# Performance work log

Hardware: AMD Instinct MI355X
Metric: run time of the kernel (lower is better)

## Reference

```python
import jax, jax.numpy as jnp
import numpy as np

NUM_HEADS = 16
HEAD_DIM = 64
PATCH_NUMS = [1, 2, 3, 4, 5, 6, 8, 10, 13, 16, 32]
MAX_SCALE_MUL = float(np.log(100.0))


def precompute_freqs_cis(dim, patch_nums, theta=10000.0):
    # Returns [L, dim//2, 2] (cos, sin) pairs; matches torch.polar construction.
    freqs = 1.0 / theta ** (np.arange(0, dim, 4)[: dim // 4].astype(np.float32) / dim)  # [dim//4]
    tx, ty = [], []
    grid = 32.0
    for p in patch_nums:
        ix, iy = np.meshgrid(np.arange(p), np.arange(p), indexing="ij")  # torch default 'ij'
        tx.append(ix.flatten().astype(np.float32) / p * grid)
        ty.append(iy.flatten().astype(np.float32) / p * grid)
    tx = np.concatenate(tx)
    ty = np.concatenate(ty)
    ang = np.concatenate([np.outer(tx, freqs), np.outer(ty, freqs)], axis=1).astype(np.float32)  # [L, dim//2]
    return np.stack([np.cos(ang), np.sin(ang)], axis=-1)  # [L, dim//2, 2]


FREQS_CIS_CROSS = jnp.asarray(precompute_freqs_cis(HEAD_DIM, [12]))  # [144, 32, 2]


def _rope(x, cis):
    # x: [B, H, S, D]; cis: [S, D//2, 2] -> complex multiply on (even, odd) pairs.
    B, H, S, D = x.shape
    xr = x.reshape(B, H, S, D // 2, 2)
    a, b = xr[..., 0], xr[..., 1]
    c = cis[..., 0][None, None]  # [1,1,S,D//2]
    d = cis[..., 1][None, None]
    return jnp.stack([a * c - b * d, a * d + b * c], axis=-1).reshape(B, H, S, D)


def setup_inputs() -> dict:
    key = jax.random.key(0)
    ks = jax.random.split(key, 6)
    B, C, Ck, Lk = 8, 1024, 1024, 144
    fc = precompute_freqs_cis(HEAD_DIM, PATCH_NUMS)
    L = fc.shape[0]  # 1704
    return {
        "x": jax.random.normal(ks[0], (B, L, C), jnp.float32),
        "y": jax.random.normal(ks[1], (B, Lk, Ck), jnp.float32),
        "freqs_cis": jnp.asarray(fc),
        "attn_bias": jax.random.normal(ks[2], (1, 1, L, Lk), jnp.float32) * 0.1,
        "Wq": jax.random.normal(ks[3], (C, C), jnp.float32) * 0.02,
        "q_bias": jnp.zeros((C,), jnp.float32),
        "Wkv": jax.random.normal(ks[4], (2 * C, Ck), jnp.float32) * 0.02,
        "v_bias": jnp.zeros((C,), jnp.float32),
        "Wproj": jax.random.normal(ks[5], (C, C), jnp.float32) * 0.02,
        "b_proj": jnp.zeros((C,), jnp.float32),
        "scale_mul": jnp.full((1, NUM_HEADS, 1, 1), np.log(4.0), jnp.float32),
    }


def reference(x, y, freqs_cis, attn_bias, Wq, q_bias, Wkv, v_bias, Wproj, b_proj, scale_mul):
    B, L, C = x.shape
    H, D = NUM_HEADS, HEAD_DIM
    Lk = y.shape[1]
    # fused QKV projections (k bias is the zero buffer)
    q = (x @ Wq.T + q_bias).reshape(B, L, H, D).transpose(0, 2, 1, 3)  # [B,H,L,D]
    kv_bias = jnp.concatenate([jnp.zeros_like(v_bias), v_bias])
    kv = (y @ Wkv.T + kv_bias).reshape(B, Lk, 2, H, D)
    k = kv[:, :, 0].transpose(0, 2, 1, 3)  # [B,H,Lk,D]
    v = kv[:, :, 1].transpose(0, 2, 1, 3)
    # attn_l2_norm path: scale = 1, per-head learned multiplier
    sm = jnp.exp(jnp.minimum(scale_mul, MAX_SCALE_MUL))  # [1,H,1,1]
    q = q / jnp.maximum(jnp.linalg.norm(q, axis=-1, keepdims=True), 1e-12) * sm
    k = k / jnp.maximum(jnp.linalg.norm(k, axis=-1, keepdims=True), 1e-12)
    # inline RoPE (cross freqs recomputed from 12x12 grid every forward in the original)
    q = _rope(q, freqs_cis)
    k = _rope(k, FREQS_CIS_CROSS)
    # manual (non-flash) masked attention, scale = 1 due to l2 norm
    logits = jnp.einsum("bhld,bhkd->bhlk", q, k) + attn_bias
    attn = jax.nn.softmax(logits, axis=-1)
    oup = jnp.einsum("bhlk,bhkd->bhld", attn, v).transpose(0, 2, 1, 3).reshape(B, L, C)
    return oup @ Wproj.T + b_proj
```

## Files before the change

### kernel.cpp

```cpp
#include <hip/hip_runtime.h>

using u16 = unsigned short;
using u32 = unsigned int;

typedef __bf16 bf16x8 __attribute__((ext_vector_type(8)));
typedef float  f32x4  __attribute__((ext_vector_type(4)));
typedef _Float16 f16;
typedef _Float16 f16x4 __attribute__((ext_vector_type(4)));
typedef _Float16 f16x8 __attribute__((ext_vector_type(8)));
typedef u16 u16x4 __attribute__((ext_vector_type(4)));

__device__ __forceinline__ float b2f(u16 u) { return __uint_as_float(((u32)u) << 16); }
__device__ __forceinline__ u16 f2b(float f) {
    u32 u = __float_as_uint(f);
    return (u16)((u + 0x7FFFu + ((u >> 16) & 1u)) >> 16);
}

__device__ __forceinline__ void async_cp16(void* lds, const void* g) {
    __builtin_amdgcn_global_load_lds(
        (const __attribute__((address_space(1))) u32*)g,
        (__attribute__((address_space(3))) u32*)lds, 16, 0, 0);
}

__global__ __launch_bounds__(256) void split_f32(const float* __restrict__ src,
                                                 u16* __restrict__ hi,
                                                 u16* __restrict__ lo, int n4) {
    int i = blockIdx.x * 256 + threadIdx.x;
    if (i >= n4) return;
    f32x4 v = reinterpret_cast<const f32x4*>(src)[i];
    u16x4 H, L;
#pragma unroll
    for (int j = 0; j < 4; j++) {
        u16 hb = f2b(v[j]);
        H[j] = hb;
        L[j] = f2b(v[j] - b2f(hb));
    }
    reinterpret_cast<u16x4*>(hi)[i] = H;
    reinterpret_cast<u16x4*>(lo)[i] = L;
}

__global__ __launch_bounds__(256) void cvt_f16(const float* __restrict__ src,
                                               f16* __restrict__ dst, int n4) {
    int i = blockIdx.x * 256 + threadIdx.x;
    if (i >= n4) return;
    f32x4 v = reinterpret_cast<const f32x4*>(src)[i];
    f16x4 h = {(f16)v[0], (f16)v[1], (f16)v[2], (f16)v[3]};
    reinterpret_cast<f16x4*>(dst)[i] = h;
}

__device__ __forceinline__ void split8(f32x4 a0, f32x4 a1, bf16x8& hi, bf16x8& lo) {
    union { bf16x8 v; u16 s[8]; } H, L;
#pragma unroll
    for (int j = 0; j < 4; j++) {
        float f = a0[j]; u16 hb = f2b(f); H.s[j] = hb;     L.s[j] = f2b(f - b2f(hb));
        float g = a1[j]; u16 gb = f2b(g); H.s[4 + j] = gb; L.s[4 + j] = f2b(g - b2f(gb));
    }
    hi = H.v; lo = L.v;
}

__global__ __launch_bounds__(512) void gemm_q(const u16* __restrict__ xhi,
                                              const u16* __restrict__ xlo,
                                              const u16* __restrict__ whi,
                                              const u16* __restrict__ wlo,
                                              const float* __restrict__ qb,
                                              const float* __restrict__ fc,
                                              const float* __restrict__ smul,
                                              f16* __restrict__ qout) {
    const int K = 1024, L = 1704;
    __shared__ u16 xs[2][2][64][64];
    int tid = threadIdx.x;
    int lane = tid & 63, wv = tid >> 6;
    int mt = blockIdx.x >> 1;
    int hg = blockIdx.x & 1;
    int h  = hg * 8 + wv;
    int lr = lane & 15, quad = lane >> 4;
    long m0 = (long)mt * 64;

    int srow = tid >> 3, scol = (tid & 7) * 8;
    const u16* g_hi = xhi + (m0 + srow) * K + scol;
    const u16* g_lo = xlo + (m0 + srow) * K + scol;
    u16* l_hi0 = &xs[0][0][srow][scol];
    u16* l_lo0 = &xs[0][1][srow][scol];
    u16* l_hi1 = &xs[1][0][srow][scol];
    u16* l_lo1 = &xs[1][1][srow][scol];

    const bf16x8* wh_p[4];
    const bf16x8* wl_p[4];
#pragma unroll
    for (int i = 0; i < 4; i++) {
        long woff = ((long)(h * 64 + i * 16 + lr)) * K;
        wh_p[i] = reinterpret_cast<const bf16x8*>(whi + woff) + quad;
        wl_p[i] = reinterpret_cast<const bf16x8*>(wlo + woff) + quad;
    }

    f32x4 acc[4][4] = {};

    async_cp16(l_hi0, g_hi);
    async_cp16(l_lo0, g_lo);
    __syncthreads();

    for (int c = 0; c < 16; c++) {
        if (c < 15) {
            const u16* gh = g_hi + (c + 1) * 64;
            const u16* gl = g_lo + (c + 1) * 64;
            if (c & 1) { async_cp16(l_hi0, gh); async_cp16(l_lo0, gl); }
            else       { async_cp16(l_hi1, gh); async_cp16(l_lo1, gl); }
        }
        int buf = c & 1;
#pragma unroll
        for (int s = 0; s < 2; s++) {
            bf16x8 AH[4], AL[4], WH[4], WL[4];
#pragma unroll
            for (int i = 0; i < 4; i++) {
                WH[i] = wh_p[i][c * 8 + s * 4];
                WL[i] = wl_p[i][c * 8 + s * 4];
            }
#pragma unroll
            for (int i = 0; i < 4; i++) {
                AH[i] = *reinterpret_cast<const bf16x8*>(&xs[buf][0][i * 16 + lr][s * 32 + quad * 8]);
                AL[i] = *reinterpret_cast<const bf16x8*>(&xs[buf][1][i * 16 + lr][s * 32 + quad * 8]);
            }
#pragma unroll
            for (int mi = 0; mi < 4; mi++)
#pragma unroll
                for (int ni = 0; ni < 4; ni++) {
                    acc[mi][ni] = __builtin_amdgcn_mfma_f32_16x16x32_bf16(AH[mi], WH[ni], acc[mi][ni], 0, 0, 0);
                    acc[mi][ni] = __builtin_amdgcn_mfma_f32_16x16x32_bf16(AL[mi], WH[ni], acc[mi][ni], 0, 0, 0);
                    acc[mi][ni] = __builtin_amdgcn_mfma_f32_16x16x32_bf16(AH[mi], WL[ni], acc[mi][ni], 0, 0, 0);
                }
        }
        __syncthreads();
    }

    float sm = __expf(fminf(smul[h], 4.6051702f));
#pragma unroll
    for (int mi = 0; mi < 4; mi++) {
#pragma unroll
        for (int r = 0; r < 4; r++) {
            long rowg = m0 + mi * 16 + quad * 4 + r;
            float v[4];
            float ss = 0.f;
#pragma unroll
            for (int ni = 0; ni < 4; ni++) {
                v[ni] = acc[mi][ni][r] + qb[h * 64 + ni * 16 + lr];
                ss += v[ni] * v[ni];
            }
            ss += __shfl_xor(ss, 1, 64); ss += __shfl_xor(ss, 2, 64);
            ss += __shfl_xor(ss, 4, 64); ss += __shfl_xor(ss, 8, 64);
            float inv = sm / fmaxf(sqrtf(ss), 1e-12f);
            int l = (int)(rowg % L);
            f16* orow = qout + rowg * 1024 + h * 64;
#pragma unroll
            for (int ni = 0; ni < 4; ni++) {
                float u = v[ni] * inv;
                int d = ni * 16 + lr;
                int j = d >> 1;
                float c = fc[(l * 32 + j) * 2];
                float s = fc[(l * 32 + j) * 2 + 1];
                float pr = __shfl_xor(u, 1, 64);
                float o = (lane & 1) ? (pr * s + u * c) : (u * c - pr * s);
                orow[d] = (f16)o;
            }
        }
    }
}

__constant__ double FREQS16[16] = {
    1.0, 0.5623413251903491, 0.31622776601683794, 0.17782794100389228,
    0.1, 0.05623413251903491, 0.03162277660168379, 0.017782794100389228,
    0.01, 0.005623413251903491, 0.0031622776601683794, 0.0017782794100389228,
    0.001, 0.0005623413251903491, 0.00031622776601683794, 0.00017782794100389228};

__global__ __launch_bounds__(256) void gemm_kv(const float* __restrict__ y,
                                               const float* __restrict__ Wkv,
                                               const float* __restrict__ vb,
                                               f16* __restrict__ khp,
                                               f16* __restrict__ klp,
                                               f16* __restrict__ vhp,
                                               f16* __restrict__ vlp) {
    const int K = 1024;
    int lane = threadIdx.x & 63, wv = threadIdx.x >> 6;
    int mt = blockIdx.x >> 3;
    int nt = (blockIdx.x & 7) * 4 + wv;
    int lr = lane & 15, quad = lane >> 4;
    long m0 = (long)mt * 64;

    const float* arow[4];
    const float* wrow[4];
#pragma unroll
    for (int i = 0; i < 4; i++) {
        arow[i] = y   + (m0 + i * 16 + lr) * K + quad * 8;
        wrow[i] = Wkv + ((long)(nt * 64 + i * 16 + lr)) * K + quad * 8;
    }

    f32x4 acc[4][4] = {};
    for (int ks = 0; ks < 32; ks++) {
        bf16x8 ah[4], al[4], wh[4], wl[4];
#pragma unroll
        for (int i = 0; i < 4; i++) {
            const float* ap = arow[i] + ks * 32;
            split8(*(const f32x4*)ap, *(const f32x4*)(ap + 4), ah[i], al[i]);
            const float* wp = wrow[i] + ks * 32;
            split8(*(const f32x4*)wp, *(const f32x4*)(wp + 4), wh[i], wl[i]);
        }
#pragma unroll
        for (int mi = 0; mi < 4; mi++)
#pragma unroll
            for (int ni = 0; ni < 4; ni++) {
                acc[mi][ni] = __builtin_amdgcn_mfma_f32_16x16x32_bf16(ah[mi], wh[ni], acc[mi][ni], 0, 0, 0);
                acc[mi][ni] = __builtin_amdgcn_mfma_f32_16x16x32_bf16(al[mi], wh[ni], acc[mi][ni], 0, 0, 0);
                acc[mi][ni] = __builtin_amdgcn_mfma_f32_16x16x32_bf16(ah[mi], wl[ni], acc[mi][ni], 0, 0, 0);
            }
    }

    bool isv = nt >= 16;
    int h = isv ? nt - 16 : nt;
#pragma unroll
    for (int mi = 0; mi < 4; mi++) {
#pragma unroll
        for (int r = 0; r < 4; r++) {
            long row = m0 + mi * 16 + quad * 4 + r;
            int b = (int)(row / 144), lk = (int)(row % 144);
            long bh = b * 16 + h;
            float v[4];
#pragma unroll
            for (int ni = 0; ni < 4; ni++)
                v[ni] = acc[mi][ni][r] + (isv ? vb[h * 64 + ni * 16 + lr] : 0.f);
            if (!isv) {
                float ss = v[0] * v[0] + v[1] * v[1] + v[2] * v[2] + v[3] * v[3];
                ss += __shfl_xor(ss, 1, 64); ss += __shfl_xor(ss, 2, 64);
                ss += __shfl_xor(ss, 4, 64); ss += __shfl_xor(ss, 8, 64);
                float inv = 1.f / fmaxf(sqrtf(ss), 1e-12f);
                f16* kh_row = khp + (bh * 144 + lk) * 64;
                f16* kl_row = klp + (bh * 144 + lk) * 64;
#pragma unroll
                for (int ni = 0; ni < 4; ni++) {
                    float u = v[ni] * inv;
                    int d = ni * 16 + lr;
                    int j = d >> 1;
                    int f = j & 15;
                    float tc = (j < 16) ? ((float)(lk / 12)) / 12.0f * 32.0f
                                        : ((float)(lk % 12)) / 12.0f * 32.0f;
                    float ang = (float)((double)tc * FREQS16[f]);
                    float c = cosf(ang), s = sinf(ang);
                    float pr = __shfl_xor(u, 1, 64);
                    float o = (lane & 1) ? (pr * s + u * c) : (u * c - pr * s);
                    f16 oh = (f16)o;
                    f16 ol = (f16)(o - (float)oh);
                    kh_row[d] = oh;
                    kl_row[d] = ol;
                }
            } else {
#pragma unroll
                for (int ni = 0; ni < 4; ni++) {
                    float val = v[ni];
                    int d = ni * 16 + lr;
                    f16 vh = (f16)val;
                    f16 vl = (f16)(val - (float)vh);
                    vhp[(bh * 64 + d) * 144 + lk] = vh;
                    vlp[(bh * 64 + d) * 144 + lk] = vl;
                }
            }
        }
    }
}

__global__ __launch_bounds__(256, 3) void attn(const f16* q,
                                               const f16* __restrict__ khp,
                                               const f16* __restrict__ klp,
                                               const f16* __restrict__ vhp,
                                               const f16* __restrict__ vlp,
                                               const float* __restrict__ abias,
                                               f16* aout) {
    const int L = 1704;
    __shared__ __align__(16) f16 ps[4][16][152];
    int tid = threadIdx.x;
    int lane = tid & 63, wv = tid >> 6;
    int lr = lane & 15, quad = lane >> 4;
    int ltile = blockIdx.x % 27;
    int bh = blockIdx.x / 27;
    int h = bh & 15, b = bh >> 4;
    int l0 = ltile * 64;
    int rows = min(64, L - l0);

    int rA = wv * 16 + lr;
    int rAc = min(rA, rows - 1);
    const f16* qrow = q + ((long)(b * L + l0 + rAc)) * 1024 + h * 64;
    f16x8 qa0 = *reinterpret_cast<const f16x8*>(qrow + quad * 8);
    f16x8 qa1 = *reinterpret_cast<const f16x8*>(qrow + 32 + quad * 8);

    const f16* khb = khp + (long)bh * (144 * 64);
    const f16* klb = klp + (long)bh * (144 * 64);

    f32x4 acc[9] = {};
#pragma unroll
    for (int t = 0; t < 9; t++) {
        const f16* k0 = khb + (t * 16 + lr) * 64 + quad * 8;
        const f16* k1 = klb + (t * 16 + lr) * 64 + quad * 8;
        f16x8 bh0 = *reinterpret_cast<const f16x8*>(k0);
        f16x8 bh1 = *reinterpret_cast<const f16x8*>(k0 + 32);
        f16x8 bl0 = *reinterpret_cast<const f16x8*>(k1);
        f16x8 bl1 = *reinterpret_cast<const f16x8*>(k1 + 32);
        acc[t] = __builtin_amdgcn_mfma_f32_16x16x32_f16(qa0, bh0, acc[t], 0, 0, 0);
        acc[t] = __builtin_amdgcn_mfma_f32_16x16x32_f16(qa1, bh1, acc[t], 0, 0, 0);
        acc[t] = __builtin_amdgcn_mfma_f32_16x16x32_f16(qa0, bl0, acc[t], 0, 0, 0);
        acc[t] = __builtin_amdgcn_mfma_f32_16x16x32_f16(qa1, bl1, acc[t], 0, 0, 0);
    }

    int rC = wv * 16 + quad * 4;
#pragma unroll
    for (int r = 0; r < 4; r++) {
        long lrow = (long)(l0 + min(rC + r, rows - 1)) * 144;
#pragma unroll
        for (int t = 0; t < 9; t++) acc[t][r] += abias[lrow + t * 16 + lr];
    }

#pragma unroll
    for (int r = 0; r < 4; r++) {
        float mx = acc[0][r];
#pragma unroll
        for (int t = 1; t < 9; t++) mx = fmaxf(mx, acc[t][r]);
        mx = fmaxf(mx, __shfl_xor(mx, 1, 64));
        mx = fmaxf(mx, __shfl_xor(mx, 2, 64));
        mx = fmaxf(mx, __shfl_xor(mx, 4, 64));
        mx = fmaxf(mx, __shfl_xor(mx, 8, 64));
        float s = 0.f;
#pragma unroll
        for (int t = 0; t < 9; t++) {
            float e = __expf(acc[t][r] - mx);
            acc[t][r] = e;
            s += e;
        }
        s += __shfl_xor(s, 1, 64);
        s += __shfl_xor(s, 2, 64);
        s += __shfl_xor(s, 4, 64);
        s += __shfl_xor(s, 8, 64);
        float inv = 1.0f / s;
#pragma unroll
        for (int t = 0; t < 9; t++)
            ps[wv][quad * 4 + r][t * 16 + lr] = (f16)(acc[t][r] * inv);
    }

    const f16* vhb = vhp + (long)bh * (64 * 144);
    const f16* vlb = vlp + (long)bh * (64 * 144);
    f32x4 oacc[4] = {};
#pragma unroll
    for (int ks = 0; ks < 5; ks++) {
        f16x8 pa = {0, 0, 0, 0, 0, 0, 0, 0};
        if (ks < 4 || quad < 2)
            pa = *reinterpret_cast<const f16x8*>(&ps[wv][lr][ks * 32 + quad * 8]);
#pragma unroll
        for (int n = 0; n < 4; n++) {
            f16x8 vh8 = {0, 0, 0, 0, 0, 0, 0, 0};
            f16x8 vl8 = {0, 0, 0, 0, 0, 0, 0, 0};
            if (ks < 4 || quad < 2) {
                const f16* vr  = vhb + (n * 16 + lr) * 144 + ks * 32 + quad * 8;
                const f16* vr2 = vlb + (n * 16 + lr) * 144 + ks * 32 + quad * 8;
                vh8 = *reinterpret_cast<const f16x8*>(vr);
                vl8 = *reinterpret_cast<const f16x8*>(vr2);
            }
            oacc[n] = __builtin_amdgcn_mfma_f32_16x16x32_f16(pa, vh8, oacc[n], 0, 0, 0);
            oacc[n] = __builtin_amdgcn_mfma_f32_16x16x32_f16(pa, vl8, oacc[n], 0, 0, 0);
        }
    }

    long ob = (long)(b * L + l0);
#pragma unroll
    for (int r = 0; r < 4; r++) {
        int rw = rC + r;
        if (rw < rows) {
            f16* ao = aout + (ob + rw) * 1024 + h * 64;
#pragma unroll
            for (int n = 0; n < 4; n++) ao[n * 16 + lr] = (f16)oacc[n][r];
        }
    }
}

__global__ __launch_bounds__(512) void gemm_proj(const f16* __restrict__ A,
                                                 const f16* __restrict__ Wh,
                                                 const float* __restrict__ bias,
                                                 float* __restrict__ out) {
    const int K = 1024;
    __shared__ f16 as[2][64][64];
    int tid = threadIdx.x;
    int lane = tid & 63, wv = tid >> 6;
    int mt = blockIdx.x >> 1;
    int cg = blockIdx.x & 1;
    int lr = lane & 15, quad = lane >> 4;
    long m0 = (long)mt * 64;
    long n0 = (long)cg * 512 + wv * 64;

    int srow = tid >> 3, scol = (tid & 7) * 8;
    const f16* g_a = A + (m0 + srow) * K + scol;
    f16* l_a0 = &as[0][srow][scol];
    f16* l_a1 = &as[1][srow][scol];

    const f16x8* wrow[4];
#pragma unroll
    for (int i = 0; i < 4; i++)
        wrow[i] = reinterpret_cast<const f16x8*>(Wh + (n0 + i * 16 + lr) * K) + quad;

    f32x4 acc[4][4] = {};

    async_cp16(l_a0, g_a);
    __syncthreads();

    for (int c = 0; c < 16; c++) {
        if (c < 15) {
            const f16* ga = g_a + (c + 1) * 64;
            if (c & 1) async_cp16(l_a0, ga);
            else       async_cp16(l_a1, ga);
        }
        int buf = c & 1;
#pragma unroll
        for (int s = 0; s < 2; s++) {
            f16x8 af[4], wf[4];
#pragma unroll
            for (int i = 0; i < 4; i++) wf[i] = wrow[i][c * 8 + s * 4];
#pragma unroll
            for (int i = 0; i < 4; i++)
                af[i] = *reinterpret_cast<const f16x8*>(&as[buf][i * 16 + lr][s * 32 + quad * 8]);
#pragma unroll
            for (int mi = 0; mi < 4; mi++)
#pragma unroll
                for (int ni = 0; ni < 4; ni++)
                    acc[mi][ni] = __builtin_amdgcn_mfma_f32_16x16x32_f16(af[mi], wf[ni], acc[mi][ni], 0, 0, 0);
        }
        __syncthreads();
    }

#pragma unroll
    for (int ni = 0; ni < 4; ni++) {
        int col = (int)n0 + ni * 16 + lr;
        float b = bias[col];
#pragma unroll
        for (int mi = 0; mi < 4; mi++) {
            long row = m0 + mi * 16 + quad * 4;
#pragma unroll
            for (int r = 0; r < 4; r++)
                out[(row + r) * 1024 + col] = acc[mi][ni][r] + b;
        }
    }
}

extern "C" void kernel_launch(void* const* d_in, const int* in_sizes, int n_in,
                              void* d_out, int out_size, void* d_ws, size_t ws_size,
                              hipStream_t stream) {
    const float* x     = (const float*)d_in[0];
    const float* y     = (const float*)d_in[1];
    const float* fc    = (const float*)d_in[2];
    const float* abias = (const float*)d_in[3];
    const float* Wq    = (const float*)d_in[4];
    const float* qb    = (const float*)d_in[5];
    const float* Wkv   = (const float*)d_in[6];
    const float* vb    = (const float*)d_in[7];
    const float* Wp    = (const float*)d_in[8];
    const float* bp    = (const float*)d_in[9];
    const float* smul  = (const float*)d_in[10];

    const long XN = 13959168L;
    const long WN = 1048576L;
    const long KVN = 1179648L;

    f16* qbuf  = (f16*)d_ws;
    u16* wq_hi = (u16*)(qbuf + XN);
    u16* wq_lo = wq_hi + WN;
    f16* wp_h  = (f16*)(wq_lo + WN);

    u16* x_hi = (u16*)d_out;
    u16* x_lo = x_hi + XN;
    f16* kh_p  = (f16*)d_out;
    f16* kl_p  = kh_p + KVN;
    f16* vth_p = kl_p + KVN;
    f16* vtl_p = vth_p + KVN;

    dim3 blk(256);
    split_f32<<<dim3((int)(XN / 4 / 256)), blk, 0, stream>>>(x, x_hi, x_lo, (int)(XN / 4));
    split_f32<<<dim3((int)(WN / 4 / 256)), blk, 0, stream>>>(Wq, wq_hi, wq_lo, (int)(WN / 4));
    cvt_f16  <<<dim3((int)(WN / 4 / 256)), blk, 0, stream>>>(Wp, wp_h, (int)(WN / 4));
    gemm_q<<<dim3(426), dim3(512), 0, stream>>>(x_hi, x_lo, wq_hi, wq_lo, qb, fc, smul, qbuf);
    gemm_kv<<<dim3(144), blk, 0, stream>>>(y, Wkv, vb, kh_p, kl_p, vth_p, vtl_p);
    attn<<<dim3(3456), blk, 0, stream>>>(qbuf, kh_p, kl_p, vth_p, vtl_p, abias, (f16*)qbuf);
    gemm_proj<<<dim3(426), dim3(512), 0, stream>>>((const f16*)qbuf, wp_h, bp, (float*)d_out);
}
```

Measured before the change: 598.2 us.

## Swizzle LDS tiles in Q/proj GEMMs and merge prep conversions into one kernel

The three fp32 conversion kernels (x and Wq split into bf16 hi/lo, Wp to fp16) are merged into one launch that picks its work by block index. The A-tile staging in gemm_q and gemm_proj now uses an XOR swizzle: each thread loads a permuted 16-byte column chunk from global memory into its LDS slot, and the MFMA fragment reads use matching swizzled offsets. The aim is to avoid LDS bank conflicts on the 64-wide rows. The K-loop is also manually split into two half-steps, so the next async copy is issued after the first weight loads rather than before them. This costs an extra XOR per thread and makes the tile layout harder to follow.

```diff
diff --git a/kernel.cpp b/kernel.cpp
--- a/kernel.cpp
+++ b/kernel.cpp
@@ -22,11 +22,7 @@
         (__attribute__((address_space(3))) u32*)lds, 16, 0, 0);
 }
 
-__global__ __launch_bounds__(256) void split_f32(const float* __restrict__ src,
-                                                 u16* __restrict__ hi,
-                                                 u16* __restrict__ lo, int n4) {
-    int i = blockIdx.x * 256 + threadIdx.x;
-    if (i >= n4) return;
+__device__ __forceinline__ void split4_store(const float* src, u16* hi, u16* lo, int i) {
     f32x4 v = reinterpret_cast<const f32x4*>(src)[i];
     u16x4 H, L;
 #pragma unroll
@@ -39,13 +35,26 @@
     reinterpret_cast<u16x4*>(lo)[i] = L;
 }
 
-__global__ __launch_bounds__(256) void cvt_f16(const float* __restrict__ src,
-                                               f16* __restrict__ dst, int n4) {
+__global__ __launch_bounds__(256) void prep(const float* __restrict__ x,
+                                            const float* __restrict__ Wq,
+                                            const float* __restrict__ Wp,
+                                            u16* __restrict__ xhi, u16* __restrict__ xlo,
+                                            u16* __restrict__ wqhi, u16* __restrict__ wqlo,
+                                            f16* __restrict__ wph,
+                                            int nx4, int nw4) {
     int i = blockIdx.x * 256 + threadIdx.x;
-    if (i >= n4) return;
-    f32x4 v = reinterpret_cast<const f32x4*>(src)[i];
-    f16x4 h = {(f16)v[0], (f16)v[1], (f16)v[2], (f16)v[3]};
-    reinterpret_cast<f16x4*>(dst)[i] = h;
+    if (i < nx4) {
+        split4_store(x, xhi, xlo, i);
+    } else if (i < nx4 + nw4) {
+        split4_store(Wq, wqhi, wqlo, i - nx4);
+    } else {
+        int k = i - nx4 - nw4;
+        if (k < nw4) {
+            f32x4 v = reinterpret_cast<const f32x4*>(Wp)[k];
+            f16x4 h = {(f16)v[0], (f16)v[1], (f16)v[2], (f16)v[3]};
+            reinterpret_cast<f16x4*>(wph)[k] = h;
+        }
+    }
 }
 
 __device__ __forceinline__ void split8(f32x4 a0, f32x4 a1, bf16x8& hi, bf16x8& lo) {
@@ -76,9 +85,11 @@
     int lr = lane & 15, quad = lane >> 4;
     long m0 = (long)mt * 64;
 
-    int srow = tid >> 3, scol = (tid & 7) * 8;
-    const u16* g_hi = xhi + (m0 + srow) * K + scol;
-    const u16* g_lo = xlo + (m0 + srow) * K + scol;
+    int srow = tid >> 3;
+    int scol = (tid & 7) * 8;
+    int slog = (((tid & 7) ^ (srow & 7))) * 8;
+    const u16* g_hi = xhi + (m0 + srow) * K + slog;
+    const u16* g_lo = xlo + (m0 + srow) * K + slog;
     u16* l_hi0 = &xs[0][0][srow][scol];
     u16* l_lo0 = &xs[0][1][srow][scol];
     u16* l_hi1 = &xs[1][0][srow][scol];
@@ -93,6 +104,9 @@
         wl_p[i] = reinterpret_cast<const bf16x8*>(wlo + woff) + quad;
     }
 
+    int sp0 = ((0 + quad) ^ (lr & 7)) * 8;
+    int sp1 = ((4 + quad) ^ (lr & 7)) * 8;
+
     f32x4 acc[4][4] = {};
 
     async_cp16(l_hi0, g_hi);
@@ -100,25 +114,47 @@
     __syncthreads();
 
     for (int c = 0; c < 16; c++) {
-        if (c < 15) {
-            const u16* gh = g_hi + (c + 1) * 64;
-            const u16* gl = g_lo + (c + 1) * 64;
-            if (c & 1) { async_cp16(l_hi0, gh); async_cp16(l_lo0, gl); }
-            else       { async_cp16(l_hi1, gh); async_cp16(l_lo1, gl); }
-        }
         int buf = c & 1;
-#pragma unroll
-        for (int s = 0; s < 2; s++) {
-            bf16x8 AH[4], AL[4], WH[4], WL[4];
+        {
+            bf16x8 WH[4], WL[4];
 #pragma unroll
             for (int i = 0; i < 4; i++) {
-                WH[i] = wh_p[i][c * 8 + s * 4];
-                WL[i] = wl_p[i][c * 8 + s * 4];
-            }
+                WH[i] = wh_p[i][c * 8];
+                WL[i] = wl_p[i][c * 8];
+            }
+            if (c < 15) {
+                const u16* gh = g_hi + (c + 1) * 64;
+                const u16* gl = g_lo + (c + 1) * 64;
+                if (c & 1) { async_cp16(l_hi0, gh); async_cp16(l_lo0, gl); }
+                else       { async_cp16(l_hi1, gh); async_cp16(l_lo1, gl); }
+            }
+            bf16x8 AH[4], AL[4];
 #pragma unroll
             for (int i = 0; i < 4; i++) {
-                AH[i] = *reinterpret_cast<const bf16x8*>(&xs[buf][0][i * 16 + lr][s * 32 + quad * 8]);
-                AL[i] = *reinterpret_cast<const bf16x8*>(&xs[buf][1][i * 16 + lr][s * 32 + quad * 8]);
+                AH[i] = *reinterpret_cast<const bf16x8*>(&xs[buf][0][i * 16 + lr][sp0]);
+                AL[i] = *reinterpret_cast<const bf16x8*>(&xs[buf][1][i * 16 + lr][sp0]);
+            }
+#pragma unroll
+            for (int mi = 0; mi < 4; mi++)
+#pragma unroll
+                for (int ni = 0; ni < 4; ni++) {
+                    acc[mi][ni] = __builtin_amdgcn_mfma_f32_16x16x32_bf16(AH[mi], WH[ni], acc[mi][ni], 0, 0, 0);
+                    acc[mi][ni] = __builtin_amdgcn_mfma_f32_16x16x32_bf16(AL[mi], WH[ni], acc[mi][ni], 0, 0, 0);
+                    acc[mi][ni] = __builtin_amdgcn_mfma_f32_16x16x32_bf16(AH[mi], WL[ni], acc[mi][ni], 0, 0, 0);
+                }
+        }
+        {
+            bf16x8 WH[4], WL[4];
+#pragma unroll
+            for (int i = 0; i < 4; i++) {
+                WH[i] = wh_p[i][c * 8 + 4];
+                WL[i] = wl_p[i][c * 8 + 4];
+            }
+            bf16x8 AH[4], AL[4];
+#pragma unroll
+            for (int i = 0; i < 4; i++) {
+                AH[i] = *reinterpret_cast<const bf16x8*>(&xs[buf][0][i * 16 + lr][sp1]);
+                AL[i] = *reinterpret_cast<const bf16x8*>(&xs[buf][1][i * 16 + lr][sp1]);
             }
 #pragma unroll
             for (int mi = 0; mi < 4; mi++)
@@ -390,8 +426,10 @@
     long m0 = (long)mt * 64;
     long n0 = (long)cg * 512 + wv * 64;
 
-    int srow = tid >> 3, scol = (tid & 7) * 8;
-    const f16* g_a = A + (m0 + srow) * K + scol;
+    int srow = tid >> 3;
+    int scol = (tid & 7) * 8;
+    int slog = (((tid & 7) ^ (srow & 7))) * 8;
+    const f16* g_a = A + (m0 + srow) * K + slog;
     f16* l_a0 = &as[0][srow][scol];
     f16* l_a1 = &as[1][srow][scol];
 
@@ -400,26 +438,43 @@
     for (int i = 0; i < 4; i++)
         wrow[i] = reinterpret_cast<const f16x8*>(Wh + (n0 + i * 16 + lr) * K) + quad;
 
+    int sp0 = ((0 + quad) ^ (lr & 7)) * 8;
+    int sp1 = ((4 + quad) ^ (lr & 7)) * 8;
+
     f32x4 acc[4][4] = {};
 
     async_cp16(l_a0, g_a);
     __syncthreads();
 
     for (int c = 0; c < 16; c++) {
-        if (c < 15) {
-            const f16* ga = g_a + (c + 1) * 64;
-            if (c & 1) async_cp16(l_a0, ga);
-            else       async_cp16(l_a1, ga);
-        }
         int buf = c & 1;
-#pragma unroll
-        for (int s = 0; s < 2; s++) {
-            f16x8 af[4], wf[4];
-#pragma unroll
-            for (int i = 0; i < 4; i++) wf[i] = wrow[i][c * 8 + s * 4];
+        {
+            f16x8 wf[4];
+#pragma unroll
+            for (int i = 0; i < 4; i++) wf[i] = wrow[i][c * 8];
+            if (c < 15) {
+                const f16* ga = g_a + (c + 1) * 64;
+                if (c & 1) async_cp16(l_a0, ga);
+                else       async_cp16(l_a1, ga);
+            }
+            f16x8 af[4];
 #pragma unroll
             for (int i = 0; i < 4; i++)
-                af[i] = *reinterpret_cast<const f16x8*>(&as[buf][i * 16 + lr][s * 32 + quad * 8]);
+                af[i] = *reinterpret_cast<const f16x8*>(&as[buf][i * 16 + lr][sp0]);
+#pragma unroll
+            for (int mi = 0; mi < 4; mi++)
+#pragma unroll
+                for (int ni = 0; ni < 4; ni++)
+                    acc[mi][ni] = __builtin_amdgcn_mfma_f32_16x16x32_f16(af[mi], wf[ni], acc[mi][ni], 0, 0, 0);
+        }
+        {
+            f16x8 wf[4];
+#pragma unroll
+            for (int i = 0; i < 4; i++) wf[i] = wrow[i][c * 8 + 4];
+            f16x8 af[4];
+#pragma unroll
+            for (int i = 0; i < 4; i++)
+                af[i] = *reinterpret_cast<const f16x8*>(&as[buf][i * 16 + lr][sp1]);
 #pragma unroll
             for (int mi = 0; mi < 4; mi++)
 #pragma unroll
@@ -474,12 +529,14 @@
     f16* vth_p = kl_p + KVN;
     f16* vtl_p = vth_p + KVN;
 
-    dim3 blk(256);
-    split_f32<<<dim3((int)(XN / 4 / 256)), blk, 0, stream>>>(x, x_hi, x_lo, (int)(XN / 4));
-    split_f32<<<dim3((int)(WN / 4 / 256)), blk, 0, stream>>>(Wq, wq_hi, wq_lo, (int)(WN / 4));
-    cvt_f16  <<<dim3((int)(WN / 4 / 256)), blk, 0, stream>>>(Wp, wp_h, (int)(WN / 4));
+    int nx4 = (int)(XN / 4);
+    int nw4 = (int)(WN / 4);
+    int prep_blocks = (nx4 + 2 * nw4) / 256;
+
+    prep<<<dim3(prep_blocks), dim3(256), 0, stream>>>(x, Wq, Wp, x_hi, x_lo,
+                                                      wq_hi, wq_lo, wp_h, nx4, nw4);
     gemm_q<<<dim3(426), dim3(512), 0, stream>>>(x_hi, x_lo, wq_hi, wq_lo, qb, fc, smul, qbuf);
-    gemm_kv<<<dim3(144), blk, 0, stream>>>(y, Wkv, vb, kh_p, kl_p, vth_p, vtl_p);
-    attn<<<dim3(3456), blk, 0, stream>>>(qbuf, kh_p, kl_p, vth_p, vtl_p, abias, (f16*)qbuf);
+    gemm_kv<<<dim3(144), dim3(256), 0, stream>>>(y, Wkv, vb, kh_p, kl_p, vth_p, vtl_p);
+    attn<<<dim3(3456), dim3(256), 0, stream>>>(qbuf, kh_p, kl_p, vth_p, vtl_p, abias, (f16*)qbuf);
     gemm_proj<<<dim3(426), dim3(512), 0, stream>>>((const f16*)qbuf, wp_h, bp, (float*)d_out);
 }
```

Measured after the change: 616.9 us. 1.03x slower.
